# Optimization experiments

Measured on AMD Instinct MI355X. Metric: run time of the kernel, lower is better.

## Reference

```python
import jax, jax.numpy as jnp
import numpy as np
import math

N_HEAD = 16
ROPE_BASE = 10000.0

def _rope_cos_sin(seq_len, head_dim, dtype):
    inv_freq = 1.0 / (ROPE_BASE ** (jnp.arange(0, head_dim, 2, dtype=jnp.float32) / head_dim))
    t = jnp.arange(seq_len, dtype=jnp.float32)
    freqs = t[:, None] * inv_freq[None, :]            # [S, D/2]
    emb = jnp.concatenate([freqs, freqs], axis=-1)     # [S, D]
    # broadcast shape [1, 1, S, D] to match q/k [B, H, S, D]
    return jnp.cos(emb)[None, None].astype(dtype), jnp.sin(emb)[None, None].astype(dtype)

def _rotate_half(x):
    x1, x2 = jnp.split(x, 2, axis=-1)
    return jnp.concatenate([-x2, x1], axis=-1)

def setup_inputs() -> dict:
    key = jax.random.key(0)
    ks = jax.random.split(key, 5)
    B, S, E = 2, 2048, 1024
    x = jax.random.normal(ks[0], (B, S, E), dtype=jnp.float32)
    init = 1.0 / math.sqrt(E)
    Wq = jax.random.normal(ks[1], (E, E), dtype=jnp.float32) * init
    Wk = jax.random.normal(ks[2], (E, E), dtype=jnp.float32) * init
    Wv = jax.random.normal(ks[3], (E, E), dtype=jnp.float32) * init
    Wo = jax.random.normal(ks[4], (E, E), dtype=jnp.float32) * init
    # causal mask: True = masked (masked_fill with -inf)
    attn_mask = jnp.triu(jnp.ones((S, S), dtype=bool), k=1)
    return {"x": x, "Wq": Wq, "Wk": Wk, "Wv": Wv, "Wo": Wo, "attn_mask": attn_mask}

def reference(x, Wq, Wk, Wv, Wo, attn_mask):
    B, S, E = x.shape
    H = N_HEAD
    D = E // H
    # projections (torch Linear: y = x @ W.T), split heads -> [B, H, S, D]
    def proj(W):
        return jnp.einsum('bse,fe->bsf', x, W).reshape(B, S, H, D).transpose(0, 2, 1, 3)
    q, k, v = proj(Wq), proj(Wk), proj(Wv)
    cos, sin = _rope_cos_sin(S, D, x.dtype)
    q = q * cos + _rotate_half(q) * sin
    k = k * cos + _rotate_half(k) * sin
    scale = 1.0 / math.sqrt(D)
    scores = jnp.einsum('bhqd,bhkd->bhqk', q, k) * scale  # [B, H, S, S]
    scores = jnp.where(attn_mask[None, None], -jnp.inf, scores)
    attn = jax.nn.softmax(scores, axis=-1)
    out = jnp.einsum('bhqk,bhkd->bhqd', attn, v)           # [B, H, S, D]
    out = out.transpose(0, 2, 1, 3).reshape(B, S, E)
    return jnp.einsum('bse,fe->bsf', out, Wo)
```

## Files before the change

kernel.cpp:

```cpp
#include <hip/hip_runtime.h>
#include <hip/hip_bf16.h>

#define NB 2
#define NH 16
#define SEQ 2048
#define HD 64
#define EMB 1024

typedef unsigned short u16;
typedef unsigned int u32;
typedef __attribute__((ext_vector_type(8))) short bf16x8;
typedef __attribute__((ext_vector_type(4))) float f32x4;
typedef __attribute__((ext_vector_type(8))) unsigned short us8;

__device__ __forceinline__ float b2f(u16 u) {
    union { unsigned int i; float f; } v; v.i = ((unsigned int)u) << 16; return v.f;
}
__device__ __forceinline__ u16 f2b(float f) {
    union { float f; unsigned int i; } v; v.f = f;
    unsigned int x = v.i;
    return (u16)((x + 0x7FFFu + ((x >> 16) & 1u)) >> 16);
}
__device__ __forceinline__ u32 pk2(float a, float b) {
    union { __hip_bfloat162 h; u32 u; } v;
    v.h = __float22bfloat162_rn(make_float2(a, b));
    return v.u;
}

__device__ __forceinline__ void gld16(const u16* g, u16* l) {
    __builtin_amdgcn_global_load_lds((const __attribute__((address_space(1))) void*)g,
                                     (__attribute__((address_space(3))) void*)l, 16, 0, 0);
}

__device__ __forceinline__ void conv8(const void* src, u16* dst, int i, int isbf16) {
    if (isbf16) {
        *reinterpret_cast<uint4*>(dst + i) =
            *reinterpret_cast<const uint4*>((const u16*)src + i);
    } else {
        const float* s = (const float*)src + i;
        float4 a = *reinterpret_cast<const float4*>(s);
        float4 b = *reinterpret_cast<const float4*>(s + 4);
        us8 v;
        v[0] = f2b(a.x); v[1] = f2b(a.y); v[2] = f2b(a.z); v[3] = f2b(a.w);
        v[4] = f2b(b.x); v[5] = f2b(b.y); v[6] = f2b(b.z); v[7] = f2b(b.w);
        *reinterpret_cast<us8*>(dst + i) = v;
    }
}

__global__ __launch_bounds__(256)
void prep_54571854463007(const void* __restrict__ x,
                         const void* __restrict__ w0, const void* __restrict__ w1,
                         const void* __restrict__ w2, const void* __restrict__ w3,
                         u16* __restrict__ xb, u16* __restrict__ dqkv,
                         u16* __restrict__ dob, int* __restrict__ flag) {
    __shared__ int cnt;
    if (threadIdx.x == 0) cnt = 0;
    __syncthreads();
    const u16 v = ((const u16*)x)[threadIdx.x];
    const int e = (v >> 7) & 0xFF;
    if (e >= 110 && e <= 135) atomicAdd(&cnt, 1);
    __syncthreads();
    const int isbf16 = (cnt >= 200) ? 1 : 0;
    const int blk = blockIdx.x;
    if (blk == 0 && threadIdx.x == 0) *flag = isbf16;
    const int NXB = (NB * SEQ * EMB) / 2048;
    if (blk < NXB) {
        conv8(x, xb, (blk * 256 + threadIdx.x) * 8, isbf16);
    } else {
        const int r = blk - NXB;
        const int seg = r >> 9;
        const int NW = EMB * EMB;
        const void* src = (seg == 0) ? w0 : (seg == 1) ? w1 : (seg == 2) ? w2 : w3;
        u16* dst = (seg < 3) ? (dqkv + (size_t)seg * NW) : dob;
        conv8(src, dst, ((r & 511) * 256 + threadIdx.x) * 8, isbf16);
    }
}

template<int OUT_MODE>
__global__ __launch_bounds__(256)
void gemm_mfma_54571854463007(const u16* __restrict__ A, const u16* __restrict__ Bw,
                              void* __restrict__ C, const int* __restrict__ flagp,
                              int M, int N, int K) {
    __shared__ __align__(16) u16 As[128 * 32];
    __shared__ __align__(16) u16 Bs[128 * 32];
    const int tid  = threadIdx.x;
    const int wave = tid >> 6, lane = tid & 63;
    const int quad = lane >> 4, fr = lane & 15;
    const int wr = (wave >> 1) * 64, wc = (wave & 1) * 64;
    const int m0 = blockIdx.y * 128, n0 = blockIdx.x * 128;
    const int r0 = tid >> 2;
    const int kc = (tid & 3) * 8;
    const f32x4 zz = {0.f, 0.f, 0.f, 0.f};
    f32x4 acc[4][4];
#pragma unroll
    for (int i = 0; i < 4; ++i)
#pragma unroll
        for (int j = 0; j < 4; ++j) acc[i][j] = zz;

    for (int k0 = 0; k0 < K; k0 += 32) {
        gld16(A  + (size_t)(m0 + r0) * K + k0 + kc,      &As[wave * 512]);
        gld16(A  + (size_t)(m0 + 64 + r0) * K + k0 + kc, &As[2048 + wave * 512]);
        gld16(Bw + (size_t)(n0 + r0) * K + k0 + kc,      &Bs[wave * 512]);
        gld16(Bw + (size_t)(n0 + 64 + r0) * K + k0 + kc, &Bs[2048 + wave * 512]);
        __syncthreads();
        bf16x8 af[4], bfr[4];
#pragma unroll
        for (int mi = 0; mi < 4; ++mi)
            af[mi] = *reinterpret_cast<const bf16x8*>(&As[(wr + mi * 16 + fr) * 32 + quad * 8]);
#pragma unroll
        for (int ni = 0; ni < 4; ++ni)
            bfr[ni] = *reinterpret_cast<const bf16x8*>(&Bs[(wc + ni * 16 + fr) * 32 + quad * 8]);
#pragma unroll
        for (int mi = 0; mi < 4; ++mi)
#pragma unroll
            for (int ni = 0; ni < 4; ++ni)
                acc[mi][ni] = __builtin_amdgcn_mfma_f32_16x16x32_bf16(af[mi], bfr[ni], acc[mi][ni], 0, 0, 0);
        __syncthreads();
    }

    if (OUT_MODE == 1) {
        const int t0 = n0 >> 10;
        if (t0 == 0) {
            const float SCL = 0.18033688011112042f;
#pragma unroll
            for (int mi = 0; mi < 4; ++mi)
#pragma unroll
                for (int ni = 0; ni < 4; ++ni)
#pragma unroll
                    for (int r = 0; r < 4; ++r) acc[mi][ni][r] *= SCL;
        }
        if (t0 < 2) {
            const float inv0 = __powf(10000.f, -(float)fr / 32.f);
            const float inv1 = __powf(10000.f, -(float)(fr + 16) / 32.f);
#pragma unroll
            for (int mi = 0; mi < 4; ++mi)
#pragma unroll
                for (int r = 0; r < 4; ++r) {
                    const int s = (m0 + wr + mi * 16 + quad * 4 + r) & (SEQ - 1);
#pragma unroll
                    for (int nl = 0; nl < 2; ++nl) {
                        float sn, cs;
                        __sincosf((float)s * (nl ? inv1 : inv0), &sn, &cs);
                        const float lo = acc[mi][nl][r], hi = acc[mi][nl + 2][r];
                        acc[mi][nl][r]     = lo * cs - hi * sn;
                        acc[mi][nl + 2][r] = hi * cs + lo * sn;
                    }
                }
        }
    }

    const int isbf16 = (OUT_MODE == 0) ? *flagp : 0;
    const size_t TS = (size_t)NB * NH * SEQ * HD;
#pragma unroll
    for (int mi = 0; mi < 4; ++mi)
#pragma unroll
        for (int ni = 0; ni < 4; ++ni)
#pragma unroll
            for (int r = 0; r < 4; ++r) {
                const int m = m0 + wr + mi * 16 + quad * 4 + r;
                const int n = n0 + wc + ni * 16 + fr;
                const float v = acc[mi][ni][r];
                if (OUT_MODE == 1) {
                    const int t = n >> 10, idx = n & 1023;
                    const int h = idx >> 6, d = idx & 63;
                    const int b = m >> 11, s = m & (SEQ - 1);
                    ((u16*)C)[t * TS + ((((size_t)b * NH + h) * SEQ + s) << 6) + d] = f2b(v);
                } else {
                    if (isbf16) ((u16*)C)[(size_t)m * N + n] = f2b(v);
                    else        ((float*)C)[(size_t)m * N + n] = v;
                }
            }
}

__global__ __launch_bounds__(256, 3)
void flash_54571854463007(const u16* __restrict__ Q, const u16* __restrict__ K,
                          const u16* __restrict__ V, u16* __restrict__ AO,
                          float* __restrict__ OP0, float* __restrict__ OP1,
                          float* __restrict__ LP0, float* __restrict__ LP1) {
    __shared__ __align__(16) u16 Kt[2 * 4096];
    __shared__ __align__(16) u16 Vt[2 * 4608];
    const int tid  = threadIdx.x;
    const int w    = tid >> 6, lane = tid & 63;
    const int quad = lane >> 4, fr = lane & 15;
    const int lin = blockIdx.x;
    const int xcd = lin & 7;
    const int r_  = lin >> 3;
    const int b4  = r_ & 3;
    const int ti  = r_ >> 2;
    int T, kt0, kt1;
    if (ti < 8)       { T = 8 + ti; kt0 = 0;  kt1 = 15; }
    else if (ti == 8) { T = 15;     kt0 = 16; kt1 = 31; }
    else if (ti == 9) { T = 7;      kt0 = 0;  kt1 = 15; }
    else {
        const int g = ti - 10, s = 7 - (g >> 1);
        if ((g & 1) == 0) { T = s + 7; kt0 = 16; kt1 = 2 * T + 1; }
        else              { T = s - 1; kt0 = 0;  kt1 = 2 * T + 1; }
    }
    const bool split = (T >= 8);
    const int bh = xcd * 4 + b4;
    const int h = bh & 15, b = bh >> 4;
    const size_t base = ((size_t)b * NH + h) * SEQ * HD;
    const int k2   = (tid & 31) * 2;
    const int key0 = (k2 & 3) * 16 + (k2 >> 2);
    const int d8   = ((tid >> 5) & 7) * 8;

    const int krs = lane >> 3;
    const int kch = ((lane & 7) ^ krs) * 8;
    const int swz = fr & 7;
    const int co0 = (quad ^ swz) * 8;
    const int co1 = ((quad + 4) ^ swz) * 8;

    const bf16x8 ones = {(short)0x3F80, (short)0x3F80, (short)0x3F80, (short)0x3F80,
                         (short)0x3F80, (short)0x3F80, (short)0x3F80, (short)0x3F80};

    const u16* qp0 = Q + base + (size_t)(T * 128 + w * 16 + fr) * HD + quad * 8;
    const bf16x8 aq0 = *reinterpret_cast<const bf16x8*>(qp0);
    const bf16x8 aq1 = *reinterpret_cast<const bf16x8*>(qp0 + 32);
    const u16* qp1 = qp0 + (size_t)64 * HD;
    const bf16x8 aq2 = *reinterpret_cast<const bf16x8*>(qp1);
    const bf16x8 aq3 = *reinterpret_cast<const bf16x8*>(qp1 + 32);

    {
        const u16* Kg = K + base + (size_t)kt0 * 64 * HD;
        gld16(Kg + (size_t)((w * 2 + 0) * 8 + krs) * HD + kch, &Kt[(w * 2 + 0) * 512]);
        gld16(Kg + (size_t)((w * 2 + 1) * 8 + krs) * HD + kch, &Kt[(w * 2 + 1) * 512]);
    }
    us8 vc0, vc1, vn0, vn1;
    {
        const u16* vs = V + base + (size_t)(kt0 * 64 + key0) * HD + d8;
        vc0 = *reinterpret_cast<const us8*>(vs);
        vc1 = *reinterpret_cast<const us8*>(vs + 16 * HD);
    }

    const f32x4 zz = {0.f, 0.f, 0.f, 0.f};
    f32x4 lacc0 = zz, lacc1 = zz;
    f32x4 oacc0[4], oacc1[4];
#pragma unroll
    for (int nt = 0; nt < 4; ++nt) { oacc0[nt] = zz; oacc1[nt] = zz; }

    for (int kt = kt0; kt <= kt1; ++kt) {
        const int buf = (kt - kt0) & 1;
        const int vb  = buf * 4608;
        const int kb  = buf * 4096;
#pragma unroll
        for (int jj = 0; jj < 8; ++jj) {
            const u32 pk = ((u32)(u16)vc1[jj] << 16) | (u32)(u16)vc0[jj];
            *reinterpret_cast<u32*>(&Vt[vb + (d8 + jj) * 72 + k2]) = pk;
        }
        __syncthreads();
        if (kt + 1 <= kt1) {
            const u16* Kg = K + base + (size_t)(kt + 1) * 64 * HD;
            const int kb1 = (buf ^ 1) * 4096;
            gld16(Kg + (size_t)((w * 2 + 0) * 8 + krs) * HD + kch, &Kt[kb1 + (w * 2 + 0) * 512]);
            gld16(Kg + (size_t)((w * 2 + 1) * 8 + krs) * HD + kch, &Kt[kb1 + (w * 2 + 1) * 512]);
            const u16* vs = V + base + (size_t)((kt + 1) * 64 + key0) * HD + d8;
            vn0 = *reinterpret_cast<const us8*>(vs);
            vn1 = *reinterpret_cast<const us8*>(vs + 16 * HD);
        }
        const int dk = kt - 2 * T;
        bf16x8 ka0[4], ka1[4];
        __builtin_amdgcn_s_setprio(1);
#pragma unroll
        for (int nt = 0; nt < 4; ++nt) {
            const int rb = kb + (nt * 16 + fr) * 64;
            ka0[nt] = *reinterpret_cast<const bf16x8*>(&Kt[rb + co0]);
            ka1[nt] = *reinterpret_cast<const bf16x8*>(&Kt[rb + co1]);
        }
        union { u32 u[4]; bf16x8 v; } p00, p01;
        {
            f32x4 sa[4];
#pragma unroll
            for (int nt = 0; nt < 4; ++nt) {
                sa[nt] = __builtin_amdgcn_mfma_f32_16x16x32_bf16(ka0[nt], aq0, zz, 0, 0, 0);
                sa[nt] = __builtin_amdgcn_mfma_f32_16x16x32_bf16(ka1[nt], aq1, sa[nt], 0, 0, 0);
            }
            __builtin_amdgcn_s_setprio(0);
            if (dk >= 0) {
#pragma unroll
                for (int nt = 0; nt < 4; ++nt)
#pragma unroll
                    for (int r = 0; r < 4; ++r)
                        if (dk * 64 + nt * 16 + quad * 4 + r > w * 16 + fr)
                            sa[nt][r] = -__builtin_inff();
            }
            u32 c01[4], c23[4];
#pragma unroll
            for (int r = 0; r < 4; ++r) {
                c01[r] = pk2(exp2f(sa[0][r]), exp2f(sa[1][r]));
                c23[r] = pk2(exp2f(sa[2][r]), exp2f(sa[3][r]));
            }
            {
                auto a = __builtin_amdgcn_permlane16_swap(c01[0], c01[2], false, false);
                auto bsw = __builtin_amdgcn_permlane32_swap(a[0], a[1], false, false);
                p00.u[0] = (u32)bsw[0]; p01.u[0] = (u32)bsw[1];
            }
            {
                auto a = __builtin_amdgcn_permlane16_swap(c23[0], c23[2], false, false);
                auto bsw = __builtin_amdgcn_permlane32_swap(a[0], a[1], false, false);
                p00.u[1] = (u32)bsw[0]; p01.u[1] = (u32)bsw[1];
            }
            {
                auto a = __builtin_amdgcn_permlane16_swap(c01[1], c01[3], false, false);
                auto bsw = __builtin_amdgcn_permlane32_swap(a[0], a[1], false, false);
                p00.u[2] = (u32)bsw[0]; p01.u[2] = (u32)bsw[1];
            }
            {
                auto a = __builtin_amdgcn_permlane16_swap(c23[1], c23[3], false, false);
                auto bsw = __builtin_amdgcn_permlane32_swap(a[0], a[1], false, false);
                p00.u[3] = (u32)bsw[0]; p01.u[3] = (u32)bsw[1];
            }
        }
        union { u32 u[4]; bf16x8 v; } p10, p11;
        {
            f32x4 sa[4];
            __builtin_amdgcn_s_setprio(1);
#pragma unroll
            for (int nt = 0; nt < 4; ++nt) {
                sa[nt] = __builtin_amdgcn_mfma_f32_16x16x32_bf16(ka0[nt], aq2, zz, 0, 0, 0);
                sa[nt] = __builtin_amdgcn_mfma_f32_16x16x32_bf16(ka1[nt], aq3, sa[nt], 0, 0, 0);
            }
            __builtin_amdgcn_s_setprio(0);
            if (dk == 1) {
#pragma unroll
                for (int nt = 0; nt < 4; ++nt)
#pragma unroll
                    for (int r = 0; r < 4; ++r)
                        if (nt * 16 + quad * 4 + r > w * 16 + fr)
                            sa[nt][r] = -__builtin_inff();
            }
            u32 c01[4], c23[4];
#pragma unroll
            for (int r = 0; r < 4; ++r) {
                c01[r] = pk2(exp2f(sa[0][r]), exp2f(sa[1][r]));
                c23[r] = pk2(exp2f(sa[2][r]), exp2f(sa[3][r]));
            }
            {
                auto a = __builtin_amdgcn_permlane16_swap(c01[0], c01[2], false, false);
                auto bsw = __builtin_amdgcn_permlane32_swap(a[0], a[1], false, false);
                p10.u[0] = (u32)bsw[0]; p11.u[0] = (u32)bsw[1];
            }
            {
                auto a = __builtin_amdgcn_permlane16_swap(c23[0], c23[2], false, false);
                auto bsw = __builtin_amdgcn_permlane32_swap(a[0], a[1], false, false);
                p10.u[1] = (u32)bsw[0]; p11.u[1] = (u32)bsw[1];
            }
            {
                auto a = __builtin_amdgcn_permlane16_swap(c01[1], c01[3], false, false);
                auto bsw = __builtin_amdgcn_permlane32_swap(a[0], a[1], false, false);
                p10.u[2] = (u32)bsw[0]; p11.u[2] = (u32)bsw[1];
            }
            {
                auto a = __builtin_amdgcn_permlane16_swap(c23[1], c23[3], false, false);
                auto bsw = __builtin_amdgcn_permlane32_swap(a[0], a[1], false, false);
                p10.u[3] = (u32)bsw[0]; p11.u[3] = (u32)bsw[1];
            }
        }
        __builtin_amdgcn_s_setprio(1);
        lacc0 = __builtin_amdgcn_mfma_f32_16x16x32_bf16(p00.v, ones, lacc0, 0, 0, 0);
        lacc0 = __builtin_amdgcn_mfma_f32_16x16x32_bf16(p01.v, ones, lacc0, 0, 0, 0);
        lacc1 = __builtin_amdgcn_mfma_f32_16x16x32_bf16(p10.v, ones, lacc1, 0, 0, 0);
        lacc1 = __builtin_amdgcn_mfma_f32_16x16x32_bf16(p11.v, ones, lacc1, 0, 0, 0);
#pragma unroll
        for (int nt = 0; nt < 4; ++nt) {
            const bf16x8 bv0 = *reinterpret_cast<const bf16x8*>(&Vt[vb + (nt * 16 + fr) * 72 + quad * 8]);
            const bf16x8 bv1 = *reinterpret_cast<const bf16x8*>(&Vt[vb + (nt * 16 + fr) * 72 + 32 + quad * 8]);
            oacc0[nt] = __builtin_amdgcn_mfma_f32_16x16x32_bf16(p00.v, bv0, oacc0[nt], 0, 0, 0);
            oacc0[nt] = __builtin_amdgcn_mfma_f32_16x16x32_bf16(p01.v, bv1, oacc0[nt], 0, 0, 0);
            oacc1[nt] = __builtin_amdgcn_mfma_f32_16x16x32_bf16(p10.v, bv0, oacc1[nt], 0, 0, 0);
            oacc1[nt] = __builtin_amdgcn_mfma_f32_16x16x32_bf16(p11.v, bv1, oacc1[nt], 0, 0, 0);
        }
        __builtin_amdgcn_s_setprio(0);
        vc0 = vn0; vc1 = vn1;
    }
    if (!split) {
#pragma unroll
        for (int r = 0; r < 4; ++r) {
            const int qr = w * 16 + quad * 4 + r;
            const float i0 = 1.0f / lacc0[r];
            const float i1 = 1.0f / lacc1[r];
            const int q0 = T * 128 + qr;
            const int q1 = T * 128 + 64 + qr;
#pragma unroll
            for (int nt = 0; nt < 4; ++nt) {
                AO[(((size_t)b * SEQ + q0) * NH + h) * HD + nt * 16 + fr] = f2b(oacc0[nt][r] * i0);
                AO[(((size_t)b * SEQ + q1) * NH + h) * HD + nt * 16 + fr] = f2b(oacc1[nt][r] * i1);
            }
        }
    } else {
        float* OP = (kt0 == 16) ? OP1 : OP0;
        float* LP = (kt0 == 16) ? LP1 : LP0;
#pragma unroll
        for (int r = 0; r < 4; ++r) {
            const int qr = w * 16 + quad * 4 + r;
            const int row0 = bh * 1024 + (T * 128 + qr) - 1024;
            const int row1 = row0 + 64;
            LP[row0] = lacc0[r];
            LP[row1] = lacc1[r];
#pragma unroll
            for (int nt = 0; nt < 4; ++nt) {
                OP[(size_t)row0 * 64 + nt * 16 + fr] = oacc0[nt][r];
                OP[(size_t)row1 * 64 + nt * 16 + fr] = oacc1[nt][r];
            }
        }
    }
}

__global__ __launch_bounds__(256)
void combine_54571854463007(const float* __restrict__ OP0, const float* __restrict__ OP1,
                            const float* __restrict__ LP0, const float* __restrict__ LP1,
                            u16* __restrict__ AO) {
    const int idx  = blockIdx.x * 256 + threadIdx.x;
    const int row  = idx >> 3;
    const int d8   = (idx & 7) * 8;
    const int bh   = row >> 10;
    const int qoff = row & 1023;
    const int h = bh & 15, b = bh >> 4;
    const int q = 1024 + qoff;
    const float4* A = reinterpret_cast<const float4*>(&OP0[(size_t)row * 64 + d8]);
    const float4* Bp = reinterpret_cast<const float4*>(&OP1[(size_t)row * 64 + d8]);
    const float4 a0 = A[0], a1 = A[1], b0 = Bp[0], b1 = Bp[1];
    const float inv = 1.0f / (LP0[row] + LP1[row]);
    us8 o;
    o[0] = f2b((a0.x + b0.x) * inv); o[1] = f2b((a0.y + b0.y) * inv);
    o[2] = f2b((a0.z + b0.z) * inv); o[3] = f2b((a0.w + b0.w) * inv);
    o[4] = f2b((a1.x + b1.x) * inv); o[5] = f2b((a1.y + b1.y) * inv);
    o[6] = f2b((a1.z + b1.z) * inv); o[7] = f2b((a1.w + b1.w) * inv);
    *reinterpret_cast<us8*>(&AO[(((size_t)b * SEQ + q) * NH + h) * HD + d8]) = o;
}

extern "C" void kernel_launch(void* const* d_in, const int* in_sizes, int n_in,
                              void* d_out, int out_size, void* d_ws, size_t ws_size,
                              hipStream_t stream) {
    (void)in_sizes; (void)n_in; (void)out_size; (void)ws_size;
    const void* x  = d_in[0];
    const void* Wq = d_in[1];
    const void* Wk = d_in[2];
    const void* Wv = d_in[3];
    const void* Wo = d_in[4];

    char* ws = (char*)d_ws;
    const size_t MB = 1024 * 1024;
    int* flag = (int*)ws;
    u16* xb   = (u16*)(ws + 64);
    u16* Wqkv = (u16*)(ws + 64 + 8 * MB);
    u16* Wob  = (u16*)(ws + 64 + 14 * MB);
    u16* Qb   = (u16*)(ws + 64 + 16 * MB);
    u16* Kb   = (u16*)(ws + 64 + 24 * MB);
    u16* Vb   = (u16*)(ws + 64 + 32 * MB);
    float* OP0 = (float*)(ws + 64 + 40 * MB);
    float* OP1 = (float*)(ws + 64 + 48 * MB);
    float* LP0 = (float*)(ws + 64 + 56 * MB);
    float* LP1 = (float*)(ws + 64 + 56 * MB + 256 * 1024);
    u16* AO   = xb;

    prep_54571854463007<<<dim3(4096), 256, 0, stream>>>(
        x, Wq, Wk, Wv, Wo, xb, Wqkv, Wob, flag);

    const int M = NB * SEQ;
    gemm_mfma_54571854463007<1><<<dim3(3 * EMB / 128, M / 128), 256, 0, stream>>>(
        xb, Wqkv, Qb, flag, M, 3 * EMB, EMB);

    flash_54571854463007<<<dim3(768), 256, 0, stream>>>(Qb, Kb, Vb, AO,
                                                        OP0, OP1, LP0, LP1);
    combine_54571854463007<<<dim3(1024), 256, 0, stream>>>(OP0, OP1, LP0, LP1, AO);

    gemm_mfma_54571854463007<0><<<dim3(EMB / 128, M / 128), 256, 0, stream>>>(
        AO, Wob, d_out, flag, M, EMB, EMB);
}
```

Baseline: 208.5 us.

## Add 256x256 eight-wave pipelined QKV GEMM with swizzled LDS and double buffering

Replaces the 128x128 single-buffered QKV projection GEMM with a new 512-thread kernel that uses 256x256 tiles, K-step 64, double-buffered LDS with an XOR swizzle, and interleaved async global-to-LDS loads between MFMA groups. It uses raw s_barrier/vmcnt waits and s_setprio so loads overlap compute. The aim is to hide load latency and raise MFMA utilisation. The trade-offs are a grid of only 12x16=192 blocks with 128 KB LDS per block, which may underfill the CUs, and hand-written wait counts that risk races. The RoPE and scale epilogue moves into the new kernel.

```diff
diff --git a/kernel.cpp b/kernel.cpp
--- a/kernel.cpp
+++ b/kernel.cpp
@@ -31,6 +31,9 @@
     __builtin_amdgcn_global_load_lds((const __attribute__((address_space(1))) void*)g,
                                      (__attribute__((address_space(3))) void*)l, 16, 0, 0);
 }
+
+#define BAR8P()  asm volatile("s_barrier" ::: "memory")
+#define VMW8P(n) asm volatile("s_waitcnt vmcnt(" #n ")" ::: "memory")
 
 __device__ __forceinline__ void conv8(const void* src, u16* dst, int i, int isbf16) {
     if (isbf16) {
@@ -76,6 +79,148 @@
     }
 }
 
+template<int MIH, int NIH>
+__device__ __forceinline__ void quad8p(const bf16x8 (&aT)[4][2], const bf16x8 (&bT)[4][2],
+                                       f32x4 (&acc)[8][4]) {
+#pragma unroll
+    for (int i = 0; i < 4; ++i)
+#pragma unroll
+        for (int j = 0; j < 2; ++j)
+#pragma unroll
+            for (int k = 0; k < 2; ++k)
+                acc[MIH * 4 + i][NIH * 2 + j] = __builtin_amdgcn_mfma_f32_16x16x32_bf16(
+                    aT[i][k], bT[NIH * 2 + j][k], acc[MIH * 4 + i][NIH * 2 + j], 0, 0, 0);
+}
+
+__device__ __forceinline__ void rd8p(const u16* Ls, int buf, int rbase, int quad, int fr,
+                                     bf16x8 (&dst)[4][2]) {
+#pragma unroll
+    for (int i = 0; i < 4; ++i) {
+        const int R  = rbase + i * 16 + fr;
+        const int rb = buf * 16384 + R * 64;
+        const int sw = R & 7;
+        dst[i][0] = *reinterpret_cast<const bf16x8*>(&Ls[rb + ((quad    ) ^ sw) * 8]);
+        dst[i][1] = *reinterpret_cast<const bf16x8*>(&Ls[rb + ((quad + 4) ^ sw) * 8]);
+    }
+}
+
+__global__ __launch_bounds__(512, 2)
+void gemm8p_54571854463007(const u16* __restrict__ A, const u16* __restrict__ Bw,
+                           u16* __restrict__ C) {
+    __shared__ __align__(16) u16 As[32768];
+    __shared__ __align__(16) u16 Bs[32768];
+    const int tid  = threadIdx.x;
+    const int w    = tid >> 6, lane = tid & 63;
+    const int quad = lane >> 4, fr = lane & 15;
+    const int wm   = w >> 2, wn = w & 3;
+    const int m0   = blockIdx.y * 256, n0 = blockIdx.x * 256;
+    const int srow = tid >> 3;
+    const int schk = ((tid & 7) ^ (srow & 7)) * 8;
+
+    auto stageU = [&](const u16* G, u16* Ls, int T, int jp, int gbase) {
+        const int buf = T & 1;
+        const int j0  = jp * 2;
+        gld16(G + (size_t)(gbase + j0 * 64      + srow) * 1024 + T * 64 + schk,
+              &Ls[buf * 16384 +  j0      * 4096 + w * 512]);
+        gld16(G + (size_t)(gbase + j0 * 64 + 64 + srow) * 1024 + T * 64 + schk,
+              &Ls[buf * 16384 + (j0 + 1) * 4096 + w * 512]);
+    };
+
+    f32x4 acc[8][4];
+    const f32x4 zz = {0.f, 0.f, 0.f, 0.f};
+#pragma unroll
+    for (int i = 0; i < 8; ++i)
+#pragma unroll
+        for (int j = 0; j < 4; ++j) acc[i][j] = zz;
+
+    stageU(A, As, 0, 0, m0); stageU(A, As, 0, 1, m0);
+    stageU(Bw, Bs, 0, 0, n0); stageU(Bw, Bs, 0, 1, n0);
+    stageU(A, As, 1, 0, m0); stageU(A, As, 1, 1, m0);
+    stageU(Bw, Bs, 1, 0, n0); stageU(Bw, Bs, 1, 1, n0);
+    VMW8P(8);
+    BAR8P();
+
+    for (int it = 0; it < 8; ++it) {
+        const int ta = 2 * it, tb = ta + 1;
+        bf16x8 aT[4][2], bT[4][2];
+        rd8p(As, 0, wm * 128, quad, fr, aT);
+        rd8p(Bs, 0, wn * 64, quad, fr, bT);
+        if (it > 0) stageU(A, As, tb, 1, m0);
+        __builtin_amdgcn_s_setprio(1); quad8p<0, 0>(aT, bT, acc); __builtin_amdgcn_s_setprio(0);
+        BAR8P();
+        if (it > 0) stageU(Bw, Bs, tb, 0, n0);
+        __builtin_amdgcn_s_setprio(1); quad8p<0, 1>(aT, bT, acc); __builtin_amdgcn_s_setprio(0);
+        BAR8P();
+        rd8p(As, 0, wm * 128 + 64, quad, fr, aT);
+        if (it > 0) stageU(Bw, Bs, tb, 1, n0);
+        __builtin_amdgcn_s_setprio(1); quad8p<1, 0>(aT, bT, acc); __builtin_amdgcn_s_setprio(0);
+        BAR8P();
+        if (it < 7) stageU(A, As, ta + 2, 0, m0);
+        __builtin_amdgcn_s_setprio(1); quad8p<1, 1>(aT, bT, acc); __builtin_amdgcn_s_setprio(0);
+        if (it < 7) { VMW8P(2); } else { VMW8P(0); }
+        BAR8P();
+        rd8p(As, 1, wm * 128, quad, fr, aT);
+        rd8p(Bs, 1, wn * 64, quad, fr, bT);
+        if (it < 7) stageU(A, As, ta + 2, 1, m0);
+        __builtin_amdgcn_s_setprio(1); quad8p<0, 0>(aT, bT, acc); __builtin_amdgcn_s_setprio(0);
+        BAR8P();
+        if (it < 7) stageU(Bw, Bs, ta + 2, 0, n0);
+        __builtin_amdgcn_s_setprio(1); quad8p<0, 1>(aT, bT, acc); __builtin_amdgcn_s_setprio(0);
+        BAR8P();
+        rd8p(As, 1, wm * 128 + 64, quad, fr, aT);
+        if (it < 7) stageU(Bw, Bs, ta + 2, 1, n0);
+        __builtin_amdgcn_s_setprio(1); quad8p<1, 0>(aT, bT, acc); __builtin_amdgcn_s_setprio(0);
+        BAR8P();
+        if (it < 7) stageU(A, As, tb + 2, 0, m0);
+        __builtin_amdgcn_s_setprio(1); quad8p<1, 1>(aT, bT, acc); __builtin_amdgcn_s_setprio(0);
+        if (it < 7) { VMW8P(2); }
+        BAR8P();
+    }
+
+    const int t0 = n0 >> 10;
+    if (t0 == 0) {
+        const float SCL = 0.18033688011112042f;
+#pragma unroll
+        for (int mi = 0; mi < 8; ++mi)
+#pragma unroll
+            for (int ni = 0; ni < 4; ++ni)
+#pragma unroll
+                for (int r = 0; r < 4; ++r) acc[mi][ni][r] *= SCL;
+    }
+    if (t0 < 2) {
+        const float inv0 = __powf(10000.f, -(float)fr / 32.f);
+        const float inv1 = __powf(10000.f, -(float)(fr + 16) / 32.f);
+#pragma unroll
+        for (int mi = 0; mi < 8; ++mi)
+#pragma unroll
+            for (int r = 0; r < 4; ++r) {
+                const int s = (m0 + wm * 128 + mi * 16 + quad * 4 + r) & (SEQ - 1);
+#pragma unroll
+                for (int nl = 0; nl < 2; ++nl) {
+                    float sn, cs;
+                    __sincosf((float)s * (nl ? inv1 : inv0), &sn, &cs);
+                    const float lo = acc[mi][nl][r], hi = acc[mi][nl + 2][r];
+                    acc[mi][nl][r]     = lo * cs - hi * sn;
+                    acc[mi][nl + 2][r] = hi * cs + lo * sn;
+                }
+            }
+    }
+    const size_t TS = (size_t)NB * NH * SEQ * HD;
+#pragma unroll
+    for (int mi = 0; mi < 8; ++mi)
+#pragma unroll
+        for (int ni = 0; ni < 4; ++ni)
+#pragma unroll
+            for (int r = 0; r < 4; ++r) {
+                const int m = m0 + wm * 128 + mi * 16 + quad * 4 + r;
+                const int n = n0 + wn * 64 + ni * 16 + fr;
+                const int t = n >> 10, idx = n & 1023;
+                const int h = idx >> 6, d = idx & 63;
+                const int b = m >> 11, s = m & (SEQ - 1);
+                C[t * TS + ((((size_t)b * NH + h) * SEQ + s) << 6) + d] = f2b(acc[mi][ni][r]);
+            }
+}
+
 template<int OUT_MODE>
 __global__ __launch_bounds__(256)
 void gemm_mfma_54571854463007(const u16* __restrict__ A, const u16* __restrict__ Bw,
@@ -118,39 +263,7 @@
         __syncthreads();
     }
 
-    if (OUT_MODE == 1) {
-        const int t0 = n0 >> 10;
-        if (t0 == 0) {
-            const float SCL = 0.18033688011112042f;
-#pragma unroll
-            for (int mi = 0; mi < 4; ++mi)
-#pragma unroll
-                for (int ni = 0; ni < 4; ++ni)
-#pragma unroll
-                    for (int r = 0; r < 4; ++r) acc[mi][ni][r] *= SCL;
-        }
-        if (t0 < 2) {
-            const float inv0 = __powf(10000.f, -(float)fr / 32.f);
-            const float inv1 = __powf(10000.f, -(float)(fr + 16) / 32.f);
-#pragma unroll
-            for (int mi = 0; mi < 4; ++mi)
-#pragma unroll
-                for (int r = 0; r < 4; ++r) {
-                    const int s = (m0 + wr + mi * 16 + quad * 4 + r) & (SEQ - 1);
-#pragma unroll
-                    for (int nl = 0; nl < 2; ++nl) {
-                        float sn, cs;
-                        __sincosf((float)s * (nl ? inv1 : inv0), &sn, &cs);
-                        const float lo = acc[mi][nl][r], hi = acc[mi][nl + 2][r];
-                        acc[mi][nl][r]     = lo * cs - hi * sn;
-                        acc[mi][nl + 2][r] = hi * cs + lo * sn;
-                    }
-                }
-        }
-    }
-
-    const int isbf16 = (OUT_MODE == 0) ? *flagp : 0;
-    const size_t TS = (size_t)NB * NH * SEQ * HD;
+    const int isbf16 = *flagp;
 #pragma unroll
     for (int mi = 0; mi < 4; ++mi)
 #pragma unroll
@@ -160,15 +273,8 @@
                 const int m = m0 + wr + mi * 16 + quad * 4 + r;
                 const int n = n0 + wc + ni * 16 + fr;
                 const float v = acc[mi][ni][r];
-                if (OUT_MODE == 1) {
-                    const int t = n >> 10, idx = n & 1023;
-                    const int h = idx >> 6, d = idx & 63;
-                    const int b = m >> 11, s = m & (SEQ - 1);
-                    ((u16*)C)[t * TS + ((((size_t)b * NH + h) * SEQ + s) << 6) + d] = f2b(v);
-                } else {
-                    if (isbf16) ((u16*)C)[(size_t)m * N + n] = f2b(v);
-                    else        ((float*)C)[(size_t)m * N + n] = v;
-                }
+                if (isbf16) ((u16*)C)[(size_t)m * N + n] = f2b(v);
+                else        ((float*)C)[(size_t)m * N + n] = v;
             }
 }
 
@@ -457,8 +563,8 @@
         x, Wq, Wk, Wv, Wo, xb, Wqkv, Wob, flag);
 
     const int M = NB * SEQ;
-    gemm_mfma_54571854463007<1><<<dim3(3 * EMB / 128, M / 128), 256, 0, stream>>>(
-        xb, Wqkv, Qb, flag, M, 3 * EMB, EMB);
+    gemm8p_54571854463007<<<dim3(3 * EMB / 256, M / 256), 512, 0, stream>>>(
+        xb, Wqkv, Qb);
 
     flash_54571854463007<<<dim3(768), 256, 0, stream>>>(Qb, Kb, Vb, AO,
                                                         OP0, OP1, LP0, LP1);
```

New measurement: 211.5 us. Within noise of the previous version (+1.4%).
